# Optimization experiments

Measured on AMD Instinct MI355X. Metric: run time of the kernel, lower is better.

## Reference

```python
import jax, jax.numpy as jnp
import numpy as np

DECAY = 0.2
TAU = float(-1.0 / np.log(DECAY))
THRESH = 0.5
DELAY = 0.1  # hidden spike events are scheduled at t + 0.1

B, E = 256, 1024
D_IN, D_H, D_OUT = 784, 400, 10
TIME_WINDOW = 64


def setup_inputs() -> dict:
    key = jax.random.key(0)
    k1, k2, k3, k4, k5, k6 = jax.random.split(key, 6)
    # chronologically sorted input spike event times per sample, in [0, time_window)
    event_times = jnp.sort(
        jax.random.uniform(k1, (B, E), dtype=jnp.float32) * TIME_WINDOW, axis=1
    )
    event_pixels = jax.random.randint(k2, (B, E), 0, D_IN, dtype=jnp.int32)
    W1 = jax.random.normal(k3, (D_H, D_IN), dtype=jnp.float32) * 0.1
    b1 = jax.random.normal(k4, (D_H,), dtype=jnp.float32) * 0.01
    W2 = jax.random.normal(k5, (D_OUT, D_H), dtype=jnp.float32) * 0.1
    b2 = jax.random.normal(k6, (D_OUT,), dtype=jnp.float32) * 0.01
    return {
        "event_times": event_times,
        "event_pixels": event_pixels,
        "W1": W1,
        "b1": b1,
        "W2": W2,
        "b2": b2,
        "time_window": TIME_WINDOW,
    }


def reference(event_times, event_pixels, W1, b1, W2, b2, time_window):
    # Event-driven LIF simulation, 784 -> 400 -> 10.
    # refractory_period == 0.0 in the source, so the refractory check never fires.
    Bn = event_times.shape[0]
    W1T = W1.T                               # [784, 400] for per-event gather
    bias1 = b1 / 784.0                       # bias contribution per input spike
    W2cols = W2.T + b2[None, :] / 400.0      # [400, 10] contribution per hidden spike
    tw = jnp.asarray(time_window, dtype=event_times.dtype)

    def hidden_event(carry, x):
        # Sequentially process one hidden neuron's (possible) spike within a
        # same-time group; resets can trigger mid-group so order matters.
        h2, counts = carry
        s, w = x                             # s: [B] bool, w: [10]
        mem_new = jnp.where(s[:, None], h2 + w[None, :], h2)
        f2 = s[:, None] & (mem_new >= THRESH)
        counts = counts + f2.astype(h2.dtype)
        h2 = jnp.where(f2, jnp.zeros_like(h2), mem_new)
        return (h2, counts), None

    def step(carry, x):
        h1, h2, counts, t1_prev, t2_prev = carry
        t, p = x                             # t: [B] float, p: [B] int
        # layer 1: decay to current time, integrate input spike, fire & reset
        h1 = h1 * jnp.exp(-(t - t1_prev) / TAU)[:, None] + W1T[p] + bias1[None, :]
        fired = h1 >= THRESH                 # [B, 400]
        h1 = jnp.where(fired, jnp.zeros_like(h1), h1)
        # layer 2: hidden events of this group all occur at t + DELAY
        th = t + DELAY
        h2 = h2 * jnp.exp(-(th - t2_prev) / TAU)[:, None]
        (h2, counts), _ = jax.lax.scan(hidden_event, (h2, counts), (fired.T, W2cols))
        return (h1, h2, counts, t, th), None

    f32 = event_times.dtype
    init = (
        jnp.zeros((Bn, 400), f32),           # h1_mem
        jnp.zeros((Bn, 10), f32),            # h2_mem
        jnp.zeros((Bn, 10), f32),            # h2_spike_counts
        jnp.zeros((Bn,), f32),               # h1 last update time
        jnp.zeros((Bn,), f32),               # h2 last update time
    )
    xs = (event_times.T, event_pixels.T)     # scan over E events chronologically
    (_, _, counts, _, _), _ = jax.lax.scan(step, init, xs)
    return counts / tw                       # [B, 10] rate-coded output
```

## Files before the change

### kernel.cpp

```cpp
#include <hip/hip_runtime.h>

#define CH 32
#define NCHUNK 32
#define NE 1024
#define DH 400
#define DIN 784
#define PF 8

#define TAUF ((float)0.6213349345596119)

__global__ void prep_transpose(const float* __restrict__ W1, float* __restrict__ W1T) {
  int idx = blockIdx.x * 256 + threadIdx.x;
  const int total = DIN * DH;
  if (idx < total) {
    int p = idx / DH;
    int j = idx - p * DH;
    W1T[idx] = W1[j * DIN + p];
  } else if (idx < total + 64) {
    W1T[idx] = 0.0f;
  }
}

#define STEP(WV)                                   \
  do {                                             \
    float mn_ = __fadd_rn(h2, (WV));               \
    bool f_ = (mn_ >= 0.5f);                       \
    cntf = f_ ? (cntf + 1.0f) : cntf;              \
    h2 = f_ ? 0.0f : mn_;                          \
  } while (0)

#define SPEC8(W0, W1, W2, W3, W4, W5, W6, W7)                                  \
  do {                                                                         \
    float q0f = __fadd_rn(h2, (W0));                                           \
    float q1f = __fadd_rn(q0f, (W1));                                          \
    float q2f = __fadd_rn(q1f, (W2));                                          \
    float q3f = __fadd_rn(q2f, (W3));                                          \
    float q4f = __fadd_rn(q3f, (W4));                                          \
    float q5f = __fadd_rn(q4f, (W5));                                          \
    float q6f = __fadd_rn(q5f, (W6));                                          \
    float q7f = __fadd_rn(q6f, (W7));                                          \
    bool anyF = (q0f >= 0.5f) | (q1f >= 0.5f) | (q2f >= 0.5f) | (q3f >= 0.5f) |\
                (q4f >= 0.5f) | (q5f >= 0.5f) | (q6f >= 0.5f) | (q7f >= 0.5f); \
    if (!anyF) {                                                               \
      h2 = q7f;                                                                \
    } else {                                                                   \
      STEP(W0); STEP(W1); STEP(W2); STEP(W3);                                  \
      STEP(W4); STEP(W5); STEP(W6); STEP(W7);                                  \
    }                                                                          \
  } while (0)

#define WSEL(PW, CW, WB)                            \
  do {                                              \
    bool c_ = (N >= (PW));                          \
    q = c_ ? (CW) : q;                              \
    r = c_ ? (N - (PW)) : r;                        \
    wb = c_ ? (WB) : wb;                            \
  } while (0)

#define RSEL64()                                                               \
  unsigned lo = (unsigned)q, hi = (unsigned)(q >> 32);                         \
  unsigned pc = (unsigned)__popc(lo);                                          \
  bool gg = r >= pc; unsigned base = gg ? 32u : 0u;                            \
  unsigned x = gg ? hi : lo; r = gg ? r - pc : r;                              \
  pc = (unsigned)__popc(x & 0xFFFFu); gg = r >= pc; base += gg ? 16u : 0u;     \
  x = gg ? (x >> 16) : (x & 0xFFFFu); r = gg ? r - pc : r;                     \
  pc = (unsigned)__popc(x & 0xFFu); gg = r >= pc; base += gg ? 8u : 0u;        \
  x = gg ? (x >> 8) : (x & 0xFFu); r = gg ? r - pc : r;                        \
  pc = (unsigned)__popc(x & 0xFu); gg = r >= pc; base += gg ? 4u : 0u;         \
  x = gg ? (x >> 4) : (x & 0xFu); r = gg ? r - pc : r;                         \
  pc = (unsigned)__popc(x & 0x3u); gg = r >= pc; base += gg ? 2u : 0u;         \
  x = gg ? (x >> 2) : (x & 0x3u); r = gg ? r - pc : r;                         \
  gg = r >= (x & 1u); base += gg ? 1u : 0u;

__device__ __forceinline__ float rl_f(float v, int l) {
  return __int_as_float(__builtin_amdgcn_readlane(__float_as_int(v), l));
}

template <bool TR>
__global__ __launch_bounds__(512, 2) void snn_main(
    const float* __restrict__ ET, const int* __restrict__ EP,
    const float* __restrict__ W1x, const float* __restrict__ b1,
    const float* __restrict__ W2, const float* __restrict__ b2,
    float* __restrict__ out) {
  __shared__ float s_W2c[401 * 16];
  __shared__ __align__(16) unsigned long long s_masksT[3][8][CH + 2];
  __shared__ float s_dec1[NE];
  __shared__ float s_dec2[NE];
  __shared__ int s_EP[NE];
  __shared__ __align__(16) int s_spklist[2][CH][64];
  __shared__ __align__(16) float s_wlistT[2][CH][16 * 20];
  __shared__ int s_spkcnt[2][CH];
  __shared__ __align__(16) int s_spk2[64];

  const int tid = threadIdx.x;
  const int b = blockIdx.x;
  const int eb = b * NE;

  for (int i = tid; i < 401 * 16; i += 512) {
    int row = i >> 4, col = i & 15;
    float v = 0.0f;
    if (row < DH && col < 10) v = __fadd_rn(W2[col * DH + row], __fdiv_rn(b2[col], 400.0f));
    s_W2c[i] = v;
  }
  for (int i = tid; i < NE; i += 512) {
    s_EP[i] = EP[eb + i];
    float t = ET[eb + i];
    float tp = (i > 0) ? ET[eb + i - 1] : 0.0f;
    s_dec1[i] = expf(__fdiv_rn(-(t - tp), TAUF));
    float th = __fadd_rn(t, 0.1f);
    float thp = (i > 0) ? __fadd_rn(tp, 0.1f) : 0.0f;
    s_dec2[i] = expf(__fdiv_rn(-(th - thp), TAUF));
  }

  const bool isProd = (tid < 448);
  const int lane = tid & 63;
  const int wv = tid >> 6;
  const bool act = (tid < DH);

  float m1 = 0.0f;
  float b1v = act ? __fdiv_rn(b1[tid < DH ? tid : DH - 1], 784.0f) : 0.0f;
  float wp[PF];

  float h2 = 0.0f, cntf = 0.0f;
  const int kk = lane & 15;

  __syncthreads();

  if (isProd) {
#pragma unroll
    for (int i = 0; i < PF; ++i) {
      int p = s_EP[i];
      wp[i] = TR ? W1x[p * DH + tid] : W1x[(tid < DH ? tid : DH - 1) * DIN + p];
    }
  } else {
#pragma unroll
    for (int i = 0; i < PF; ++i) wp[i] = 0.0f;
  }

  for (int it = 0; it <= NCHUNK + 1; ++it) {
    if (isProd) {
      if (it < NCHUNK) {
        const int mb = it % 3;
        const int gbase = it * CH;
        float decv = s_dec1[(gbase + lane) & (NE - 1)];
        int epv = s_EP[(gbase + 8 + lane) & (NE - 1)];
        unsigned long long balPrev = 0ull;
#pragma unroll
        for (int e = 0; e < CH; ++e) {
          float dv = rl_f(decv, e);
          float mm = __fmul_rn(m1, dv);
          mm = __fadd_rn(mm, wp[e & (PF - 1)]);
          mm = __fadd_rn(mm, b1v);
          bool fired = act && (mm >= 0.5f);
          unsigned long long bal = __ballot(fired);
          m1 = fired ? 0.0f : mm;
          if ((e & 1) == 0) {
            balPrev = bal;
          } else if (lane == 0) {
            ulonglong2 pr; pr.x = balPrev; pr.y = bal;
            *reinterpret_cast<ulonglong2*>(&s_masksT[mb][wv][e - 1]) = pr;
          }
          int pn = __builtin_amdgcn_readlane(epv, e);
          wp[e & (PF - 1)] =
              TR ? W1x[pn * DH + tid] : W1x[(tid < DH ? tid : DH - 1) * DIN + pn];
        }
      }
      if (it >= 1 && it <= NCHUNK) {
        const int c = it - 1;
        const int mb = c % 3;
        const int lb = c & 1;
        for (int e = wv; e < CH; e += 7) {
          uint2 mw = *reinterpret_cast<const uint2*>(&s_masksT[mb][lane & 7][e]);
          unsigned long long c0 =
              ((unsigned long long)(unsigned)__builtin_amdgcn_readlane(mw.y, 0) << 32) |
              (unsigned)__builtin_amdgcn_readlane(mw.x, 0);
          unsigned long long c1 =
              ((unsigned long long)(unsigned)__builtin_amdgcn_readlane(mw.y, 1) << 32) |
              (unsigned)__builtin_amdgcn_readlane(mw.x, 1);
          unsigned long long c2 =
              ((unsigned long long)(unsigned)__builtin_amdgcn_readlane(mw.y, 2) << 32) |
              (unsigned)__builtin_amdgcn_readlane(mw.x, 2);
          unsigned long long c3 =
              ((unsigned long long)(unsigned)__builtin_amdgcn_readlane(mw.y, 3) << 32) |
              (unsigned)__builtin_amdgcn_readlane(mw.x, 3);
          unsigned long long c4 =
              ((unsigned long long)(unsigned)__builtin_amdgcn_readlane(mw.y, 4) << 32) |
              (unsigned)__builtin_amdgcn_readlane(mw.x, 4);
          unsigned long long c5 =
              ((unsigned long long)(unsigned)__builtin_amdgcn_readlane(mw.y, 5) << 32) |
              (unsigned)__builtin_amdgcn_readlane(mw.x, 5);
          unsigned long long c6 =
              ((unsigned long long)(unsigned)__builtin_amdgcn_readlane(mw.y, 6) << 32) |
              (unsigned)__builtin_amdgcn_readlane(mw.x, 6);
          unsigned P1 = (unsigned)__popcll(c0);
          unsigned P2 = P1 + (unsigned)__popcll(c1);
          unsigned P3 = P2 + (unsigned)__popcll(c2);
          unsigned P4 = P3 + (unsigned)__popcll(c3);
          unsigned P5 = P4 + (unsigned)__popcll(c4);
          unsigned P6 = P5 + (unsigned)__popcll(c5);
          unsigned total = P6 + (unsigned)__popcll(c6);
          unsigned N = (unsigned)lane;
          unsigned long long q = c0;
          unsigned r = N, wb = 0;
          WSEL(P1, c1, 64);  WSEL(P2, c2, 128); WSEL(P3, c3, 192);
          WSEL(P4, c4, 256); WSEL(P5, c5, 320); WSEL(P6, c6, 384);
          RSEL64();
          int j = (int)(wb + base);
          j = (N < total) ? j : DH;
          s_spklist[lb][e][lane] = j;
          if (lane == 0) s_spkcnt[lb][e] = (int)total;
#pragma unroll
          for (int p = 0; p < 2; ++p) {
            int sl = p * 4 + (lane >> 4);
            int js = __builtin_amdgcn_ds_bpermute(sl << 2, j);
            float w = s_W2c[js * 16 + (lane & 15)];
            s_wlistT[lb][e][(lane & 15) * 20 + sl] = w;
          }
          if (total > 8) {
#pragma unroll
            for (int p = 2; p < 4; ++p) {
              int sl = p * 4 + (lane >> 4);
              int js = __builtin_amdgcn_ds_bpermute(sl << 2, j);
              float w = s_W2c[js * 16 + (lane & 15)];
              s_wlistT[lb][e][(lane & 15) * 20 + sl] = w;
            }
          }
        }
      }
    } else {
      if (it >= 2) {
        const int c = it - 2;
        const int lb = c & 1;
        const int mb = c % 3;
        const int gb2 = c * CH;
        int cntv = s_spkcnt[lb][lane & 31];
        float d2v = s_dec2[gb2 + (lane & 31)];

        auto loadEvt = [&](int ee, int& tot, float& cdv, float (&w)[16]) {
          tot = __builtin_amdgcn_readlane(cntv, ee);
          cdv = rl_f(d2v, ee);
          const float4* wrow = reinterpret_cast<const float4*>(&s_wlistT[lb][ee][kk * 20]);
          float4 a = wrow[0], b4 = wrow[1];
          w[0] = a.x; w[1] = a.y; w[2] = a.z; w[3] = a.w;
          w[4] = b4.x; w[5] = b4.y; w[6] = b4.z; w[7] = b4.w;
          if (tot > 8) {
            float4 c4 = wrow[2], d4 = wrow[3];
            w[8] = c4.x; w[9] = c4.y; w[10] = c4.z; w[11] = c4.w;
            w[12] = d4.x; w[13] = d4.y; w[14] = d4.z; w[15] = d4.w;
          }
        };
        auto procEvt = [&](int e, int tot, float cdv, float (&w)[16]) {
          h2 = __fmul_rn(h2, cdv);
          if (tot > 0) {
            SPEC8(w[0], w[1], w[2], w[3], w[4], w[5], w[6], w[7]);
            if (tot > 8) {
              SPEC8(w[8], w[9], w[10], w[11], w[12], w[13], w[14], w[15]);
            }
            if (tot > 16) {
              int lim = tot < 64 ? tot : 64;
              for (int dn = 16; dn < lim; dn += 8) {
                const int4* sp = (const int4*)(&s_spklist[lb][e][dn]);
                int4 ja = sp[0], jb = sp[1];
                float v0 = s_W2c[ja.x * 16 + kk];
                float v1 = s_W2c[ja.y * 16 + kk];
                float v2 = s_W2c[ja.z * 16 + kk];
                float v3 = s_W2c[ja.w * 16 + kk];
                float v4 = s_W2c[jb.x * 16 + kk];
                float v5 = s_W2c[jb.y * 16 + kk];
                float v6 = s_W2c[jb.z * 16 + kk];
                float v7 = s_W2c[jb.w * 16 + kk];
                SPEC8(v0, v1, v2, v3, v4, v5, v6, v7);
              }
              if (tot > 64) {
                uint2 mw = *reinterpret_cast<const uint2*>(&s_masksT[mb][lane & 7][e]);
                unsigned long long c0 =
                    ((unsigned long long)(unsigned)__builtin_amdgcn_readlane(mw.y, 0) << 32) |
                    (unsigned)__builtin_amdgcn_readlane(mw.x, 0);
                unsigned long long c1 =
                    ((unsigned long long)(unsigned)__builtin_amdgcn_readlane(mw.y, 1) << 32) |
                    (unsigned)__builtin_amdgcn_readlane(mw.x, 1);
                unsigned long long c2 =
                    ((unsigned long long)(unsigned)__builtin_amdgcn_readlane(mw.y, 2) << 32) |
                    (unsigned)__builtin_amdgcn_readlane(mw.x, 2);
                unsigned long long c3 =
                    ((unsigned long long)(unsigned)__builtin_amdgcn_readlane(mw.y, 3) << 32) |
                    (unsigned)__builtin_amdgcn_readlane(mw.x, 3);
                unsigned long long c4 =
                    ((unsigned long long)(unsigned)__builtin_amdgcn_readlane(mw.y, 4) << 32) |
                    (unsigned)__builtin_amdgcn_readlane(mw.x, 4);
                unsigned long long c5 =
                    ((unsigned long long)(unsigned)__builtin_amdgcn_readlane(mw.y, 5) << 32) |
                    (unsigned)__builtin_amdgcn_readlane(mw.x, 5);
                unsigned long long c6 =
                    ((unsigned long long)(unsigned)__builtin_amdgcn_readlane(mw.y, 6) << 32) |
                    (unsigned)__builtin_amdgcn_readlane(mw.x, 6);
                unsigned P1 = (unsigned)__popcll(c0);
                unsigned P2 = P1 + (unsigned)__popcll(c1);
                unsigned P3 = P2 + (unsigned)__popcll(c2);
                unsigned P4 = P3 + (unsigned)__popcll(c3);
                unsigned P5 = P4 + (unsigned)__popcll(c4);
                unsigned P6 = P5 + (unsigned)__popcll(c5);
                for (int done = 64; done < tot; done += 64) {
                  unsigned N = (unsigned)(done + lane);
                  unsigned long long q = c0;
                  unsigned r = N, wb = 0;
                  WSEL(P1, c1, 64);  WSEL(P2, c2, 128); WSEL(P3, c3, 192);
                  WSEL(P4, c4, 256); WSEL(P5, c5, 320); WSEL(P6, c6, 384);
                  RSEL64();
                  int j = (int)(wb + base);
                  j = (N < (unsigned)tot) ? j : DH;
                  s_spk2[lane] = j;
                  int cnt = tot - done; cnt = cnt > 64 ? 64 : cnt;
                  int nb2 = (cnt + 7) >> 3;
                  for (int bb = 0; bb < nb2; ++bb) {
                    const int4* sp = (const int4*)(s_spk2 + bb * 8);
                    int4 ja = sp[0], jb = sp[1];
                    float v0 = s_W2c[ja.x * 16 + kk];
                    float v1 = s_W2c[ja.y * 16 + kk];
                    float v2 = s_W2c[ja.z * 16 + kk];
                    float v3 = s_W2c[ja.w * 16 + kk];
                    float v4 = s_W2c[jb.x * 16 + kk];
                    float v5 = s_W2c[jb.y * 16 + kk];
                    float v6 = s_W2c[jb.z * 16 + kk];
                    float v7 = s_W2c[jb.w * 16 + kk];
                    SPEC8(v0, v1, v2, v3, v4, v5, v6, v7);
                  }
                }
              }
            }
          }
        };

        int totA, totB; float cdA, cdB; float wA[16], wB[16];
        loadEvt(0, totA, cdA, wA);
        for (int e = 0; e < CH; e += 2) {
          loadEvt(e + 1, totB, cdB, wB);
          procEvt(e, totA, cdA, wA);
          if (e + 2 < CH) loadEvt(e + 2, totA, cdA, wA);
          procEvt(e + 1, totB, cdB, wB);
        }
      }
    }
    __syncthreads();
  }

  if (!isProd && lane < 10) out[b * 10 + lane] = __fmul_rn(cntf, 0.015625f);
}

extern "C" void kernel_launch(void* const* d_in, const int* in_sizes, int n_in,
                              void* d_out, int out_size, void* d_ws, size_t ws_size,
                              hipStream_t stream) {
  const float* ET = (const float*)d_in[0];
  const int* EP = (const int*)d_in[1];
  const float* W1 = (const float*)d_in[2];
  const float* b1 = (const float*)d_in[3];
  const float* W2 = (const float*)d_in[4];
  const float* b2 = (const float*)d_in[5];
  float* out = (float*)d_out;

  const size_t need = (size_t)(DIN * DH + 64) * sizeof(float);
  if (ws_size >= need) {
    float* W1T = (float*)d_ws;
    hipLaunchKernelGGL(prep_transpose, dim3((DIN * DH + 64 + 255) / 256), dim3(256), 0, stream,
                       W1, W1T);
    hipLaunchKernelGGL((snn_main<true>), dim3(256), dim3(512), 0, stream,
                       ET, EP, W1T, b1, W2, b2, out);
  } else {
    hipLaunchKernelGGL((snn_main<false>), dim3(256), dim3(512), 0, stream,
                       ET, EP, W1, b1, W2, b2, out);
  }
}
```

Before: 244.7 us.

## Split mask extraction onto dedicated wavefronts with 1024-thread blocks

After: 262.1 us. +7.1%, slower.

```diff
diff --git a/kernel.cpp b/kernel.cpp
--- a/kernel.cpp
+++ b/kernel.cpp
@@ -6,6 +6,7 @@
 #define DH 400
 #define DIN 784
 #define PF 8
+#define NTHR 1024
 
 #define TAUF ((float)0.6213349345596119)
 
@@ -72,12 +73,36 @@
   x = gg ? (x >> 2) : (x & 0x3u); r = gg ? r - pc : r;                         \
   gg = r >= (x & 1u); base += gg ? 1u : 0u;
 
+#define LOADMASKS(MB, E)                                                       \
+  uint2 mw = *reinterpret_cast<const uint2*>(&s_masksT[MB][lane & 7][E]);      \
+  unsigned long long c0 =                                                      \
+      ((unsigned long long)(unsigned)__builtin_amdgcn_readlane(mw.y, 0) << 32) |\
+      (unsigned)__builtin_amdgcn_readlane(mw.x, 0);                            \
+  unsigned long long c1 =                                                      \
+      ((unsigned long long)(unsigned)__builtin_amdgcn_readlane(mw.y, 1) << 32) |\
+      (unsigned)__builtin_amdgcn_readlane(mw.x, 1);                            \
+  unsigned long long c2 =                                                      \
+      ((unsigned long long)(unsigned)__builtin_amdgcn_readlane(mw.y, 2) << 32) |\
+      (unsigned)__builtin_amdgcn_readlane(mw.x, 2);                            \
+  unsigned long long c3 =                                                      \
+      ((unsigned long long)(unsigned)__builtin_amdgcn_readlane(mw.y, 3) << 32) |\
+      (unsigned)__builtin_amdgcn_readlane(mw.x, 3);                            \
+  unsigned long long c4 =                                                      \
+      ((unsigned long long)(unsigned)__builtin_amdgcn_readlane(mw.y, 4) << 32) |\
+      (unsigned)__builtin_amdgcn_readlane(mw.x, 4);                            \
+  unsigned long long c5 =                                                      \
+      ((unsigned long long)(unsigned)__builtin_amdgcn_readlane(mw.y, 5) << 32) |\
+      (unsigned)__builtin_amdgcn_readlane(mw.x, 5);                            \
+  unsigned long long c6 =                                                      \
+      ((unsigned long long)(unsigned)__builtin_amdgcn_readlane(mw.y, 6) << 32) |\
+      (unsigned)__builtin_amdgcn_readlane(mw.x, 6);
+
 __device__ __forceinline__ float rl_f(float v, int l) {
   return __int_as_float(__builtin_amdgcn_readlane(__float_as_int(v), l));
 }
 
 template <bool TR>
-__global__ __launch_bounds__(512, 2) void snn_main(
+__global__ __launch_bounds__(NTHR, 4) void snn_main(
     const float* __restrict__ ET, const int* __restrict__ EP,
     const float* __restrict__ W1x, const float* __restrict__ b1,
     const float* __restrict__ W2, const float* __restrict__ b2,
@@ -96,13 +121,13 @@
   const int b = blockIdx.x;
   const int eb = b * NE;
 
-  for (int i = tid; i < 401 * 16; i += 512) {
+  for (int i = tid; i < 401 * 16; i += NTHR) {
     int row = i >> 4, col = i & 15;
     float v = 0.0f;
     if (row < DH && col < 10) v = __fadd_rn(W2[col * DH + row], __fdiv_rn(b2[col], 400.0f));
     s_W2c[i] = v;
   }
-  for (int i = tid; i < NE; i += 512) {
+  for (int i = tid; i < NE; i += NTHR) {
     s_EP[i] = EP[eb + i];
     float t = ET[eb + i];
     float tp = (i > 0) ? ET[eb + i - 1] : 0.0f;
@@ -112,9 +137,11 @@
     s_dec2[i] = expf(__fdiv_rn(-(th - thp), TAUF));
   }
 
-  const bool isProd = (tid < 448);
   const int lane = tid & 63;
   const int wv = tid >> 6;
+  const bool isL1 = (wv < 7);
+  const bool isEx = (wv >= 7 && wv < 15);
+  const bool isCons = (wv == 15);
   const bool act = (tid < DH);
 
   float m1 = 0.0f;
@@ -126,7 +153,7 @@
 
   __syncthreads();
 
-  if (isProd) {
+  if (isL1) {
 #pragma unroll
     for (int i = 0; i < PF; ++i) {
       int p = s_EP[i];
@@ -138,7 +165,7 @@
   }
 
   for (int it = 0; it <= NCHUNK + 1; ++it) {
-    if (isProd) {
+    if (isL1) {
       if (it < NCHUNK) {
         const int mb = it % 3;
         const int gbase = it * CH;
@@ -165,33 +192,16 @@
               TR ? W1x[pn * DH + tid] : W1x[(tid < DH ? tid : DH - 1) * DIN + pn];
         }
       }
+    } else if (isEx) {
       if (it >= 1 && it <= NCHUNK) {
         const int c = it - 1;
         const int mb = c % 3;
         const int lb = c & 1;
-        for (int e = wv; e < CH; e += 7) {
-          uint2 mw = *reinterpret_cast<const uint2*>(&s_masksT[mb][lane & 7][e]);
-          unsigned long long c0 =
-              ((unsigned long long)(unsigned)__builtin_amdgcn_readlane(mw.y, 0) << 32) |
-              (unsigned)__builtin_amdgcn_readlane(mw.x, 0);
-          unsigned long long c1 =
-              ((unsigned long long)(unsigned)__builtin_amdgcn_readlane(mw.y, 1) << 32) |
-              (unsigned)__builtin_amdgcn_readlane(mw.x, 1);
-          unsigned long long c2 =
-              ((unsigned long long)(unsigned)__builtin_amdgcn_readlane(mw.y, 2) << 32) |
-              (unsigned)__builtin_amdgcn_readlane(mw.x, 2);
-          unsigned long long c3 =
-              ((unsigned long long)(unsigned)__builtin_amdgcn_readlane(mw.y, 3) << 32) |
-              (unsigned)__builtin_amdgcn_readlane(mw.x, 3);
-          unsigned long long c4 =
-              ((unsigned long long)(unsigned)__builtin_amdgcn_readlane(mw.y, 4) << 32) |
-              (unsigned)__builtin_amdgcn_readlane(mw.x, 4);
-          unsigned long long c5 =
-              ((unsigned long long)(unsigned)__builtin_amdgcn_readlane(mw.y, 5) << 32) |
-              (unsigned)__builtin_amdgcn_readlane(mw.x, 5);
-          unsigned long long c6 =
-              ((unsigned long long)(unsigned)__builtin_amdgcn_readlane(mw.y, 6) << 32) |
-              (unsigned)__builtin_amdgcn_readlane(mw.x, 6);
+        const int e0 = (wv - 7) * 4;
+#pragma unroll
+        for (int k = 0; k < 4; ++k) {
+          const int e = e0 + k;
+          LOADMASKS(mb, e);
           unsigned P1 = (unsigned)__popcll(c0);
           unsigned P2 = P1 + (unsigned)__popcll(c1);
           unsigned P3 = P2 + (unsigned)__popcll(c2);
@@ -228,7 +238,7 @@
         }
       }
     } else {
-      if (it >= 2) {
+      if (isCons && it >= 2) {
         const int c = it - 2;
         const int lb = c & 1;
         const int mb = c % 3;
@@ -272,28 +282,7 @@
                 SPEC8(v0, v1, v2, v3, v4, v5, v6, v7);
               }
               if (tot > 64) {
-                uint2 mw = *reinterpret_cast<const uint2*>(&s_masksT[mb][lane & 7][e]);
-                unsigned long long c0 =
-                    ((unsigned long long)(unsigned)__builtin_amdgcn_readlane(mw.y, 0) << 32) |
-                    (unsigned)__builtin_amdgcn_readlane(mw.x, 0);
-                unsigned long long c1 =
-                    ((unsigned long long)(unsigned)__builtin_amdgcn_readlane(mw.y, 1) << 32) |
-                    (unsigned)__builtin_amdgcn_readlane(mw.x, 1);
-                unsigned long long c2 =
-                    ((unsigned long long)(unsigned)__builtin_amdgcn_readlane(mw.y, 2) << 32) |
-                    (unsigned)__builtin_amdgcn_readlane(mw.x, 2);
-                unsigned long long c3 =
-                    ((unsigned long long)(unsigned)__builtin_amdgcn_readlane(mw.y, 3) << 32) |
-                    (unsigned)__builtin_amdgcn_readlane(mw.x, 3);
-                unsigned long long c4 =
-                    ((unsigned long long)(unsigned)__builtin_amdgcn_readlane(mw.y, 4) << 32) |
-                    (unsigned)__builtin_amdgcn_readlane(mw.x, 4);
-                unsigned long long c5 =
-                    ((unsigned long long)(unsigned)__builtin_amdgcn_readlane(mw.y, 5) << 32) |
-                    (unsigned)__builtin_amdgcn_readlane(mw.x, 5);
-                unsigned long long c6 =
-                    ((unsigned long long)(unsigned)__builtin_amdgcn_readlane(mw.y, 6) << 32) |
-                    (unsigned)__builtin_amdgcn_readlane(mw.x, 6);
+                LOADMASKS(mb, e);
                 unsigned P1 = (unsigned)__popcll(c0);
                 unsigned P2 = P1 + (unsigned)__popcll(c1);
                 unsigned P3 = P2 + (unsigned)__popcll(c2);
@@ -344,7 +333,7 @@
     __syncthreads();
   }
 
-  if (!isProd && lane < 10) out[b * 10 + lane] = __fmul_rn(cntf, 0.015625f);
+  if (isCons && lane < 10) out[b * 10 + lane] = __fmul_rn(cntf, 0.015625f);
 }
 
 extern "C" void kernel_launch(void* const* d_in, const int* in_sizes, int n_in,
@@ -363,10 +352,10 @@
     float* W1T = (float*)d_ws;
     hipLaunchKernelGGL(prep_transpose, dim3((DIN * DH + 64 + 255) / 256), dim3(256), 0, stream,
                        W1, W1T);
-    hipLaunchKernelGGL((snn_main<true>), dim3(256), dim3(512), 0, stream,
+    hipLaunchKernelGGL((snn_main<true>), dim3(256), dim3(NTHR), 0, stream,
                        ET, EP, W1T, b1, W2, b2, out);
   } else {
-    hipLaunchKernelGGL((snn_main<false>), dim3(256), dim3(512), 0, stream,
+    hipLaunchKernelGGL((snn_main<false>), dim3(256), dim3(NTHR), 0, stream,
                        ET, EP, W1, b1, W2, b2, out);
   }
 }
```
